# Kernel optimization log

Hardware: AMD Instinct MI355X
Metric: run time of the kernel (lower is better)

Reference implementation:

```python
import jax, jax.numpy as jnp
import numpy as np

EPS = 1e-5  # BatchNorm eps (torch default)


def _coords():
    # coord_tensor[i] = [(i//5 - 2)/2, (i%5 - 2)/2] for 5x5 grid of 25 objects
    i = jnp.arange(25)
    return jnp.stack([(i // 5 - 2) / 2.0, (i % 5 - 2) / 2.0], axis=-1).astype(jnp.float32)


def _conv_bn(x, w, b, gamma, beta):
    # conv stride2 pad1 -> relu -> batchnorm (training-mode batch stats, as torch module default)
    y = jax.lax.conv_general_dilated(x, w, (2, 2), ((1, 1), (1, 1)),
                                     dimension_numbers=('NCHW', 'OIHW', 'NCHW'))
    y = jax.nn.relu(y + b[None, :, None, None])
    m = y.mean(axis=(0, 2, 3), keepdims=True)
    v = y.var(axis=(0, 2, 3), keepdims=True)
    return gamma[None, :, None, None] * (y - m) * jax.lax.rsqrt(v + EPS) + beta[None, :, None, None]


def setup_inputs() -> dict:
    key = jax.random.key(0)
    ks = iter(jax.random.split(key, 64))
    def rn(shape, scale=0.05):
        return jax.random.normal(next(ks), shape, jnp.float32) * scale
    B = 256
    inp = {
        'x': jax.random.normal(next(ks), (B, 3, 80, 80), jnp.float32),
        'qst': jax.random.normal(next(ks), (B, 11), jnp.float32),
    }
    for l, (ci, co) in enumerate([(3, 24), (24, 24), (24, 24), (24, 24)], 1):
        inp[f'cw{l}'] = rn((co, ci, 3, 3))
        inp[f'cb{l}'] = jnp.zeros((co,), jnp.float32)
        inp[f'bg{l}'] = jnp.ones((co,), jnp.float32)
        inp[f'bb{l}'] = jnp.zeros((co,), jnp.float32)
    for l, (di, do) in enumerate([(63, 256), (256, 256), (256, 256), (256, 256)], 1):
        inp[f'gw{l}'] = rn((di, do))
        inp[f'gb{l}'] = jnp.zeros((do,), jnp.float32)
    for l, (di, do) in enumerate([(256, 256), (256, 256), (256, 10)], 1):
        inp[f'fw{l}'] = rn((di, do))
        inp[f'fb{l}'] = jnp.zeros((do,), jnp.float32)
    return inp


def _forward(x, qst, cw1, cb1, bg1, bb1, cw2, cb2, bg2, bb2,
             cw3, cb3, bg3, bb3, cw4, cb4, bg4, bb4,
             gw1, gb1, gw2, gb2, gw3, gb3, gw4, gb4,
             fw1, fb1, fw2, fb2, fw3, fb3):
    B = x.shape[0]
    # Convolution stack: (B,3,80,80) -> (B,24,5,5)
    h = _conv_bn(x, cw1, cb1, bg1, bb1)
    h = _conv_bn(h, cw2, cb2, bg2, bb2)
    h = _conv_bn(h, cw3, cb3, bg3, bb3)
    h = _conv_bn(h, cw4, cb4, bg4, bb4)
    # Objects: (B,24,25) -> (B,25,24) -> concat coords -> (B,25,26)
    obj = h.reshape(B, 24, 25).transpose(0, 2, 1)
    obj = jnp.concatenate([obj, jnp.broadcast_to(_coords()[None], (B, 25, 2))], axis=-1)
    # Pairwise broadcast-concat: cat([x_i, x_j, qst]) with x_i[b,p,q]=obj[b,q], x_j[b,p,q]=obj[b,p]
    xi = jnp.broadcast_to(obj[:, None, :, :], (B, 25, 25, 26))
    xj = jnp.broadcast_to(obj[:, :, None, :], (B, 25, 25, 26))
    qb = jnp.broadcast_to(qst[:, None, None, :], (B, 25, 25, 11))
    pairs = jnp.concatenate([xi, xj, qb], axis=-1).reshape(B, 625, 63)
    g = jax.nn.relu(pairs @ gw1 + gb1)
    g = jax.nn.relu(g @ gw2 + gb2)
    g = jax.nn.relu(g @ gw3 + gb3)
    g = jax.nn.relu(g @ gw4 + gb4).sum(axis=1)  # (B,256)
    # f_phi (dropout treated as identity for a deterministic reference)
    f = jax.nn.relu(g @ fw1 + fb1)
    f = jax.nn.relu(f @ fw2 + fb2)
    logits = f @ fw3 + fb3
    return jax.nn.log_softmax(logits, axis=1)


def reference(x, qst, cw1, cb1, bg1, bb1, cw2, cb2, bg2, bb2,
              cw3, cb3, bg3, bb3, cw4, cb4, bg4, bb4,
              gw1, gb1, gw2, gb2, gw3, gb3, gw4, gb4,
              fw1, fb1, fw2, fb2, fw3, fb3):
    return _forward(x, qst, cw1, cb1, bg1, bb1, cw2, cb2, bg2, bb2,
                    cw3, cb3, bg3, bb3, cw4, cb4, bg4, bb4,
                    gw1, gb1, gw2, gb2, gw3, gb3, gw4, gb4,
                    fw1, fb1, fw2, fb2, fw3, fb3)
```

## Files before the change

kernel.cpp:

```cpp
#include <hip/hip_runtime.h>
#include <hip/hip_bf16.h>


typedef __attribute__((ext_vector_type(8))) short short8;
typedef __attribute__((ext_vector_type(4))) float floatx4;

__device__ __forceinline__ unsigned short f2bf(float v){
  union { float f; unsigned int u; } c; c.f = v;
  unsigned int u = c.u;
  u += 0x7FFFu + ((u >> 16) & 1u);
  return (unsigned short)(u >> 16);
}

__global__ __launch_bounds__(256) void prep_w_zero(
    const float* __restrict__ gw2, const float* __restrict__ gw3,
    const float* __restrict__ gw4, unsigned short* __restrict__ wf,
    float* __restrict__ stats)
{
  const int bid = blockIdx.x, tid = threadIdx.x;
  if (bid == 0){ for (int j = tid; j < 1536; j += 256) stats[j] = 0.f; }
  const int w = bid >> 8;
  const float* gw = (w == 0) ? gw2 : (w == 1) ? gw3 : gw4;
  const int idx = (bid & 255)*256 + tid;
  const int i = idx & 7, lane = (idx >> 3) & 63, t = (idx >> 9) & 15, kk = idx >> 13;
  const int k = kk*32 + (lane >> 4)*8 + i;
  const int c = t*16 + (lane & 15);
  wf[w*65536 + idx] = f2bf(gw[k*256 + c]);
}

template<int CI, int COG, int PX>
__global__ __launch_bounds__(256) void conv_px(
    const float* __restrict__ in,
    const float* __restrict__ stats_in, const float* __restrict__ gprev,
    const float* __restrict__ bprev, float invN,
    const float* __restrict__ cw, const float* __restrict__ cb,
    float* __restrict__ out, float* __restrict__ stats_out,
    int H, int W, int OH, int OW)
{
  const int co0 = blockIdx.y * COG;
  __shared__ float ssm[2*CI];
  __shared__ float psum[4][COG], psum2[4][COG];
  const int tid = threadIdx.x;
  if (tid < CI){
    if (stats_in){
      float S = 0.f, S2 = 0.f;
      #pragma unroll
      for (int sh = 0; sh < 8; sh++){ S += stats_in[sh*48 + tid]; S2 += stats_in[sh*48 + 24 + tid]; }
      const float mean = S*invN;
      const float var  = S2*invN - mean*mean;
      const float rs   = rsqrtf(var + 1e-5f);
      const float sc   = gprev[tid]*rs;
      ssm[tid] = sc; ssm[CI + tid] = bprev[tid] - mean*sc;
    } else { ssm[tid] = 1.f; ssm[CI + tid] = 0.f; }
  }
  __syncthreads();
  const int nw = OW / PX;
  const int idx = blockIdx.x*256 + tid;
  const int pw = idx % nw; const int t2 = idx / nw;
  const int oh = t2 % OH;  const int b  = t2 / OH;
  const int ow0 = pw * PX;
  const float* cwb = cw + co0*CI*9;
  constexpr int NC = 2*PX + 1;
  float acc[PX][COG];
  #pragma unroll
  for (int j = 0; j < PX; j++)
    #pragma unroll
    for (int g = 0; g < COG; g++) acc[j][g] = cb[co0 + g];

  #pragma unroll 1
  for (int ci = 0; ci < CI; ci++){
    const float* ip = in + ((long)(b*CI + ci))*H*W;
    const float sc = ssm[ci], sh2 = ssm[CI + ci];
    float v[3][NC];
    #pragma unroll
    for (int kh = 0; kh < 3; kh++){
      const int ih = oh*2 - 1 + kh;
      const bool hok = (ih >= 0);
      #pragma unroll
      for (int c9 = 0; c9 < NC; c9++){
        const int iw = ow0*2 - 1 + c9;
        const bool ok = hok & (iw >= 0);
        const float raw = ip[ok ? ih*W + iw : 0];
        v[kh][c9] = ok ? raw*sc + sh2 : 0.f;
      }
    }
    #pragma unroll
    for (int g = 0; g < COG; g++){
      #pragma unroll
      for (int kh = 0; kh < 3; kh++){
        const float w0 = cwb[(g*CI + ci)*9 + kh*3 + 0];
        const float w1 = cwb[(g*CI + ci)*9 + kh*3 + 1];
        const float w2 = cwb[(g*CI + ci)*9 + kh*3 + 2];
        #pragma unroll
        for (int j = 0; j < PX; j++)
          acc[j][g] += v[kh][2*j]*w0 + v[kh][2*j+1]*w1 + v[kh][2*j+2]*w2;
      }
    }
  }

  const int wave = tid >> 6, lane = tid & 63;
  float s[COG], s2[COG];
  #pragma unroll
  for (int g = 0; g < COG; g++){
    float tmp[PX], a = 0.f, a2 = 0.f;
    #pragma unroll
    for (int j = 0; j < PX; j++){
      tmp[j] = fmaxf(acc[j][g], 0.f);
      a += tmp[j]; a2 += tmp[j]*tmp[j];
    }
    float* op = &out[(((long)b*24 + co0 + g)*OH + oh)*OW + ow0];
    if constexpr (PX == 4) *(float4*)op = make_float4(tmp[0], tmp[1], tmp[2], tmp[3]);
    else if constexpr (PX == 2) *(float2*)op = make_float2(tmp[0], tmp[1]);
    else op[0] = tmp[0];
    s[g] = a; s2[g] = a2;
  }
  #pragma unroll
  for (int g = 0; g < COG; g++){
    float a = s[g], a2 = s2[g];
    for (int off = 32; off; off >>= 1){ a += __shfl_down(a, off); a2 += __shfl_down(a2, off); }
    if (lane == 0){ psum[wave][g] = a; psum2[wave][g] = a2; }
  }
  __syncthreads();
  if (tid < COG){
    const float S  = psum[0][tid] + psum[1][tid] + psum[2][tid] + psum[3][tid];
    const float S2 = psum2[0][tid] + psum2[1][tid] + psum2[2][tid] + psum2[3][tid];
    const int sh = blockIdx.x & 7;
    atomicAdd(&stats_out[sh*48 + co0 + tid],      S);
    atomicAdd(&stats_out[sh*48 + 24 + co0 + tid], S2);
  }
}

__global__ __launch_bounds__(512) void g_mega(
    const float* __restrict__ y4, const float* __restrict__ stats4,
    const float* __restrict__ bg4, const float* __restrict__ bb4,
    const float* __restrict__ qst, const float* __restrict__ gw1,
    const float* __restrict__ gb1,
    const unsigned short* __restrict__ Wf,
    const float* __restrict__ gb2, const float* __restrict__ gb3, const float* __restrict__ gb4,
    const float* __restrict__ fw1, const float* __restrict__ fb1,
    const float* __restrict__ fw2, const float* __restrict__ fb2,
    const float* __restrict__ fw3, const float* __restrict__ fb3,
    float* __restrict__ out)
{
  __shared__ __align__(16) short act[128*256];
  __shared__ __align__(16) float A_lds[25][260];
  __shared__ __align__(16) float Bm_lds[25][260];
  __shared__ float obj[25][26];
  __shared__ float ssum[48];
  __shared__ float ssm[48];
  __shared__ float scratch[512];
  __shared__ __align__(16) float bufA[256], bufB[256];
  __shared__ float lg[10];

  const int b = blockIdx.x, tid = threadIdx.x;
  char* actB = (char*)act;
  const int wave = tid >> 6, lane = tid & 63;
  const int lmod = lane & 15, ldiv = lane >> 4;
  const int wm = wave >> 2, wn = wave & 3;

  if (tid < 48){
    float S = 0.f;
    #pragma unroll
    for (int sh = 0; sh < 8; sh++) S += stats4[sh*48 + tid];
    ssum[tid] = S;
  }
  __syncthreads();
  if (tid < 24){
    const float mean = ssum[tid]*(1.f/6400.f);
    const float var  = ssum[24 + tid]*(1.f/6400.f) - mean*mean;
    const float rs   = rsqrtf(var + 1e-5f);
    const float sc   = bg4[tid]*rs;
    ssm[tid] = sc; ssm[24 + tid] = bb4[tid] - mean*sc;
  }
  __syncthreads();
  for (int j = tid; j < 600; j += 512){
    const int q = j/24, c = j%24;
    obj[q][c] = ssm[c]*y4[((long)(b*24 + c))*25 + q] + ssm[24 + c];
  }
  if (tid < 50){
    const int q = tid >> 1;
    obj[q][24 + (tid & 1)] = (tid & 1) ? (float)(q%5 - 2)*0.5f : (float)(q/5 - 2)*0.5f;
  }
  __syncthreads();
  {
    const int n = tid & 255, half = tid >> 8;
    float wa[26], wb[26];
    #pragma unroll
    for (int c = 0; c < 26; c++){ wa[c] = gw1[c*256 + n]; wb[c] = gw1[(26 + c)*256 + n]; }
    float qv = gb1[n];
    #pragma unroll
    for (int j = 0; j < 11; j++) qv += qst[b*11 + j]*gw1[(52 + j)*256 + n];
    const int q0 = half ? 13 : 0, q1 = half ? 25 : 13;
    for (int q = q0; q < q1; q++){
      float a = qv, bm = 0.f;
      #pragma unroll
      for (int c = 0; c < 26; c++){ const float o = obj[q][c]; a += o*wa[c]; bm += o*wb[c]; }
      A_lds[q][n] = a; Bm_lds[q][n] = bm;
    }
  }
  __syncthreads();

  float gsum = 0.f;
  for (int blk = 0; blk < 5; blk++){
    const int rowbase = blk * 128;
    const int nrows = min(128, 625 - rowbase);
    {
      const int r  = tid >> 2;
      const int q4 = tid & 3;
      if (r < nrows){
        const int row = rowbase + r;
        const float* ap = &A_lds [row % 25][q4*4];
        const float* bp = &Bm_lds[row / 25][q4*4];
        #pragma unroll
        for (int j = 0; j < 16; j++){
          const int c = j*16;
          floatx4 av = *(const floatx4*)(ap + c);
          floatx4 bv = *(const floatx4*)(bp + c);
          unsigned int p0 = (unsigned int)f2bf(fmaxf(av.x+bv.x, 0.f))
                          | ((unsigned int)f2bf(fmaxf(av.y+bv.y, 0.f)) << 16);
          unsigned int p1 = (unsigned int)f2bf(fmaxf(av.z+bv.z, 0.f))
                          | ((unsigned int)f2bf(fmaxf(av.w+bv.w, 0.f)) << 16);
          const int byte = (r*512 + (c + q4*4)*2) ^ ((r & 7) << 4);
          *(uint2*)(actB + byte) = make_uint2(p0, p1);
        }
      } else {
        #pragma unroll
        for (int j = 0; j < 16; j++){
          const int byte = (r*512 + (j*16 + q4*4)*2) ^ ((r & 7) << 4);
          *(uint2*)(actB + byte) = make_uint2(0u, 0u);
        }
      }
    }
    __syncthreads();

    for (int L = 0; L < 3; L++){
      floatx4 acc[4][4];
      #pragma unroll
      for (int m = 0; m < 4; m++)
        #pragma unroll
        for (int n = 0; n < 4; n++)
          acc[m][n] = (floatx4){0.f,0.f,0.f,0.f};
      const short8* wlayer = (const short8*)Wf + (long)L*8192;
      #pragma unroll
      for (int kk = 0; kk < 8; kk++){
        short8 bf[4];
        #pragma unroll
        for (int n = 0; n < 4; n++)
          bf[n] = wlayer[(kk*16 + wn*4 + n)*64 + lane];
        short8 af[4];
        #pragma unroll
        for (int m = 0; m < 4; m++){
          const int arow  = wm*64 + m*16 + lmod;
          const int abyte = (arow*512 + kk*64 + ldiv*16) ^ ((arow & 7) << 4);
          af[m] = *(const short8*)(actB + abyte);
        }
        #pragma unroll
        for (int n = 0; n < 4; n++)
          #pragma unroll
          for (int m = 0; m < 4; m++)
            acc[m][n] = __builtin_amdgcn_mfma_f32_16x16x32_bf16(af[m], bf[n], acc[m][n], 0, 0, 0);
      }

      if (L < 2){
        const float* bias = (L == 0) ? gb2 : gb3;
        __syncthreads();
        #pragma unroll
        for (int n = 0; n < 4; n++){
          const int c = (wn*4 + n)*16 + lmod;
          const float bv = bias[c];
          #pragma unroll
          for (int m = 0; m < 4; m++){
            #pragma unroll
            for (int i = 0; i < 4; i++){
              const int row = wm*64 + m*16 + ldiv*4 + i;
              const float v = fmaxf(acc[m][n][i] + bv, 0.f);
              const int byte = (row*512 + c*2) ^ ((row & 7) << 4);
              *(short*)(actB + byte) = (short)f2bf(v);
            }
          }
        }
        __syncthreads();
      } else {
        __syncthreads();
        #pragma unroll
        for (int n = 0; n < 4; n++){
          const int c = (wn*4 + n)*16 + lmod;
          const float bv = gb4[c];
          float sv = 0.f;
          #pragma unroll
          for (int m = 0; m < 4; m++){
            #pragma unroll
            for (int i = 0; i < 4; i++){
              const int row = wm*64 + m*16 + ldiv*4 + i;
              const float v = fmaxf(acc[m][n][i] + bv, 0.f);
              if (row < nrows) sv += v;
            }
          }
          sv += __shfl_xor(sv, 16);
          sv += __shfl_xor(sv, 32);
          if (ldiv == 0) scratch[wm*256 + c] = sv;
        }
        __syncthreads();
        if (tid < 256) gsum += scratch[tid] + scratch[256 + tid];
      }
    }
  }

  if (tid < 256) bufA[tid] = gsum;
  __syncthreads();
  const int n = tid & 255;
  float acc = 0.f;
  if (tid < 256){
    acc = fb1[n];
    const float4* pa = (const float4*)bufA;
    #pragma unroll 8
    for (int k4 = 0; k4 < 64; k4++){
      const float4 a = pa[k4];
      acc += a.x*fw1[(k4*4 + 0)*256 + n];
      acc += a.y*fw1[(k4*4 + 1)*256 + n];
      acc += a.z*fw1[(k4*4 + 2)*256 + n];
      acc += a.w*fw1[(k4*4 + 3)*256 + n];
    }
    bufB[n] = fmaxf(acc, 0.f);
  }
  __syncthreads();
  if (tid < 256){
    acc = fb2[n];
    const float4* pb = (const float4*)bufB;
    #pragma unroll 8
    for (int k4 = 0; k4 < 64; k4++){
      const float4 a = pb[k4];
      acc += a.x*fw2[(k4*4 + 0)*256 + n];
      acc += a.y*fw2[(k4*4 + 1)*256 + n];
      acc += a.z*fw2[(k4*4 + 2)*256 + n];
      acc += a.w*fw2[(k4*4 + 3)*256 + n];
    }
  }
  __syncthreads();
  if (tid < 256) bufA[n] = fmaxf(acc, 0.f);
  __syncthreads();
  if (tid < 10){
    float a3 = fb3[tid];
    for (int k = 0; k < 256; k++) a3 += bufA[k]*fw3[k*10 + tid];
    lg[tid] = a3;
  }
  __syncthreads();
  if (tid < 10){
    float m = lg[0];
    #pragma unroll
    for (int j = 1; j < 10; j++) m = fmaxf(m, lg[j]);
    float s = 0.f;
    #pragma unroll
    for (int j = 0; j < 10; j++) s += expf(lg[j] - m);
    out[b*10 + tid] = lg[tid] - m - logf(s);
  }
}

extern "C" void kernel_launch(void* const* d_in, const int* in_sizes, int n_in,
                              void* d_out, int out_size, void* d_ws, size_t ws_size,
                              hipStream_t stream)
{
  const float* x   = (const float*)d_in[0];
  const float* qst = (const float*)d_in[1];
  const float* cw1 = (const float*)d_in[2];
  const float* cb1 = (const float*)d_in[3];
  const float* bg1 = (const float*)d_in[4];
  const float* bb1 = (const float*)d_in[5];
  const float* cw2 = (const float*)d_in[6];
  const float* cb2 = (const float*)d_in[7];
  const float* bg2 = (const float*)d_in[8];
  const float* bb2 = (const float*)d_in[9];
  const float* cw3 = (const float*)d_in[10];
  const float* cb3 = (const float*)d_in[11];
  const float* bg3 = (const float*)d_in[12];
  const float* bb3 = (const float*)d_in[13];
  const float* cw4 = (const float*)d_in[14];
  const float* cb4 = (const float*)d_in[15];
  const float* bg4 = (const float*)d_in[16];
  const float* bb4 = (const float*)d_in[17];
  const float* gw1 = (const float*)d_in[18];
  const float* gb1 = (const float*)d_in[19];
  const float* gw2 = (const float*)d_in[20];
  const float* gb2 = (const float*)d_in[21];
  const float* gw3 = (const float*)d_in[22];
  const float* gb3 = (const float*)d_in[23];
  const float* gw4 = (const float*)d_in[24];
  const float* gb4 = (const float*)d_in[25];
  const float* fw1 = (const float*)d_in[26];
  const float* fb1 = (const float*)d_in[27];
  const float* fw2 = (const float*)d_in[28];
  const float* fb2 = (const float*)d_in[29];
  const float* fw3 = (const float*)d_in[30];
  const float* fb3 = (const float*)d_in[31];

  float* wsf    = (float*)d_ws;
  unsigned short* Wf = (unsigned short*)(wsf + 65728);
  float* stats  = wsf + 164032;
  float* y1     = wsf + 240832;
  float* y2     = wsf + 10071232;
  float* y3     = wsf + 12528832;
  float* y4     = wsf + 13143232;

  prep_w_zero<<<768, 256, 0, stream>>>(gw2, gw3, gw4, Wf, stats);
  conv_px<3,8,4><<<dim3(400,3), 256, 0, stream>>>(x, nullptr, nullptr, nullptr, 0.f,
                                               cw1, cb1, y1, stats + 0, 80,80,40,40);
  conv_px<24,8,4><<<dim3(100,3), 256, 0, stream>>>(y1, stats + 0, bg1, bb1, 1.f/409600.f,
                                               cw2, cb2, y2, stats + 384, 40,40,20,20);
  conv_px<24,8,2><<<dim3(50,3), 256, 0, stream>>>(y2, stats + 384, bg2, bb2, 1.f/102400.f,
                                               cw3, cb3, y3, stats + 768, 20,20,10,10);
  conv_px<24,8,1><<<dim3(25,3), 256, 0, stream>>>(y3, stats + 768, bg3, bb3, 1.f/25600.f,
                                              cw4, cb4, y4, stats + 1152, 10,10,5,5);
  g_mega<<<256, 512, 0, stream>>>(y4, stats + 1152, bg4, bb4, qst, gw1, gb1, Wf,
                                  gb2, gb3, gb4, fw1, fb1, fw2, fb2, fw3, fb3,
                                  (float*)d_out);
}
```

Measured before the change: 288.9 us.

## Fuse weight prep into conv1 and replace atomic BN stats with per-block partials

```diff
diff --git a/kernel.cpp b/kernel.cpp
--- a/kernel.cpp
+++ b/kernel.cpp
@@ -12,46 +12,124 @@
   return (unsigned short)(u >> 16);
 }
 
-__global__ __launch_bounds__(256) void prep_w_zero(
+__global__ __launch_bounds__(256) void conv1_fat(
     const float* __restrict__ gw2, const float* __restrict__ gw3,
     const float* __restrict__ gw4, unsigned short* __restrict__ wf,
-    float* __restrict__ stats)
+    const float* __restrict__ x, const float* __restrict__ cw1,
+    const float* __restrict__ cb1,
+    float* __restrict__ out, float* __restrict__ pstats1)
 {
   const int bid = blockIdx.x, tid = threadIdx.x;
-  if (bid == 0){ for (int j = tid; j < 1536; j += 256) stats[j] = 0.f; }
-  const int w = bid >> 8;
-  const float* gw = (w == 0) ? gw2 : (w == 1) ? gw3 : gw4;
-  const int idx = (bid & 255)*256 + tid;
-  const int i = idx & 7, lane = (idx >> 3) & 63, t = (idx >> 9) & 15, kk = idx >> 13;
-  const int k = kk*32 + (lane >> 4)*8 + i;
-  const int c = t*16 + (lane & 15);
-  wf[w*65536 + idx] = f2bf(gw[k*256 + c]);
+  if (bid < 768){
+    const int w = bid >> 8;
+    const float* gw = (w == 0) ? gw2 : (w == 1) ? gw3 : gw4;
+    const int idx = (bid & 255)*256 + tid;
+    const int i = idx & 7, lane = (idx >> 3) & 63, t = (idx >> 9) & 15, kk = idx >> 13;
+    const int k = kk*32 + (lane >> 4)*8 + i;
+    const int c = t*16 + (lane & 15);
+    wf[w*65536 + idx] = f2bf(gw[k*256 + c]);
+    return;
+  }
+  __shared__ float psum[4][8], psum2[4][8];
+  const int cb = bid - 768;
+  const int grp = cb / 400, xb = cb % 400;
+  const int co0 = grp * 8;
+  const int idx = xb*256 + tid;
+  const int pw = idx % 10; const int t2 = idx / 10;
+  const int oh = t2 % 40;  const int b  = t2 / 40;
+  const int ow0 = pw * 4;
+  const float* cwb = cw1 + co0*3*9;
+  float acc[4][8];
+  #pragma unroll
+  for (int j = 0; j < 4; j++)
+    #pragma unroll
+    for (int g = 0; g < 8; g++) acc[j][g] = cb1[co0 + g];
+  #pragma unroll
+  for (int ci = 0; ci < 3; ci++){
+    const float* ip = x + ((long)(b*3 + ci))*6400;
+    float v[3][9];
+    #pragma unroll
+    for (int kh = 0; kh < 3; kh++){
+      const int ih = oh*2 - 1 + kh;
+      const bool hok = (ih >= 0);
+      #pragma unroll
+      for (int c9 = 0; c9 < 9; c9++){
+        const int iw = ow0*2 - 1 + c9;
+        const bool ok = hok & (iw >= 0);
+        v[kh][c9] = ok ? ip[ok ? ih*80 + iw : 0] : 0.f;
+      }
+    }
+    #pragma unroll
+    for (int g = 0; g < 8; g++){
+      #pragma unroll
+      for (int kh = 0; kh < 3; kh++){
+        const float w0 = cwb[(g*3 + ci)*9 + kh*3 + 0];
+        const float w1 = cwb[(g*3 + ci)*9 + kh*3 + 1];
+        const float w2 = cwb[(g*3 + ci)*9 + kh*3 + 2];
+        #pragma unroll
+        for (int j = 0; j < 4; j++)
+          acc[j][g] += v[kh][2*j]*w0 + v[kh][2*j+1]*w1 + v[kh][2*j+2]*w2;
+      }
+    }
+  }
+  const int wave = tid >> 6, lane = tid & 63;
+  float s[8], s2[8];
+  #pragma unroll
+  for (int g = 0; g < 8; g++){
+    float tmp[4], a = 0.f, a2 = 0.f;
+    #pragma unroll
+    for (int j = 0; j < 4; j++){
+      tmp[j] = fmaxf(acc[j][g], 0.f);
+      a += tmp[j]; a2 += tmp[j]*tmp[j];
+    }
+    *(float4*)&out[(((long)b*24 + co0 + g)*40 + oh)*40 + ow0] =
+        make_float4(tmp[0], tmp[1], tmp[2], tmp[3]);
+    s[g] = a; s2[g] = a2;
+  }
+  #pragma unroll
+  for (int g = 0; g < 8; g++){
+    float a = s[g], a2 = s2[g];
+    for (int off = 32; off; off >>= 1){ a += __shfl_down(a, off); a2 += __shfl_down(a2, off); }
+    if (lane == 0){ psum[wave][g] = a; psum2[wave][g] = a2; }
+  }
+  __syncthreads();
+  if (tid < 8){
+    pstats1[(co0 + tid)*400 + xb]      = psum[0][tid] + psum[1][tid] + psum[2][tid] + psum[3][tid];
+    pstats1[(24 + co0 + tid)*400 + xb] = psum2[0][tid] + psum2[1][tid] + psum2[2][tid] + psum2[3][tid];
+  }
 }
 
-template<int CI, int COG, int PX>
+template<int CI, int COG, int PX, int NIN, int NOUT>
 __global__ __launch_bounds__(256) void conv_px(
-    const float* __restrict__ in,
-    const float* __restrict__ stats_in, const float* __restrict__ gprev,
-    const float* __restrict__ bprev, float invN,
+    const float* __restrict__ in, const float* __restrict__ pst_in,
+    const float* __restrict__ gprev, const float* __restrict__ bprev, float invN,
     const float* __restrict__ cw, const float* __restrict__ cb,
-    float* __restrict__ out, float* __restrict__ stats_out,
+    float* __restrict__ out, float* __restrict__ pst_out,
     int H, int W, int OH, int OW)
 {
   const int co0 = blockIdx.y * COG;
+  __shared__ float psub[48][5];
   __shared__ float ssm[2*CI];
   __shared__ float psum[4][COG], psum2[4][COG];
   const int tid = threadIdx.x;
-  if (tid < CI){
-    if (stats_in){
-      float S = 0.f, S2 = 0.f;
-      #pragma unroll
-      for (int sh = 0; sh < 8; sh++){ S += stats_in[sh*48 + tid]; S2 += stats_in[sh*48 + 24 + tid]; }
-      const float mean = S*invN;
-      const float var  = S2*invN - mean*mean;
-      const float rs   = rsqrtf(var + 1e-5f);
-      const float sc   = gprev[tid]*rs;
-      ssm[tid] = sc; ssm[CI + tid] = bprev[tid] - mean*sc;
-    } else { ssm[tid] = 1.f; ssm[CI + tid] = 0.f; }
+  if (tid < 240){
+    const int c = tid / 5, sub = tid % 5;
+    constexpr int chunk = NIN / 5;
+    const float* p = pst_in + c*NIN + sub*chunk;
+    float S0 = 0.f, S1 = 0.f;
+    #pragma unroll 2
+    for (int j = 0; j < chunk; j += 2){ S0 += p[j]; S1 += p[j+1]; }
+    psub[c][sub] = S0 + S1;
+  }
+  __syncthreads();
+  if (tid < 24){
+    const float Sm  = psub[tid][0] + psub[tid][1] + psub[tid][2] + psub[tid][3] + psub[tid][4];
+    const float S2m = psub[24+tid][0] + psub[24+tid][1] + psub[24+tid][2] + psub[24+tid][3] + psub[24+tid][4];
+    const float mean = Sm*invN;
+    const float var  = S2m*invN - mean*mean;
+    const float rs   = rsqrtf(var + 1e-5f);
+    const float sc   = gprev[tid]*rs;
+    ssm[tid] = sc; ssm[CI + tid] = bprev[tid] - mean*sc;
   }
   __syncthreads();
   const int nw = OW / PX;
@@ -122,16 +200,13 @@
   }
   __syncthreads();
   if (tid < COG){
-    const float S  = psum[0][tid] + psum[1][tid] + psum[2][tid] + psum[3][tid];
-    const float S2 = psum2[0][tid] + psum2[1][tid] + psum2[2][tid] + psum2[3][tid];
-    const int sh = blockIdx.x & 7;
-    atomicAdd(&stats_out[sh*48 + co0 + tid],      S);
-    atomicAdd(&stats_out[sh*48 + 24 + co0 + tid], S2);
+    pst_out[(co0 + tid)*NOUT + blockIdx.x]      = psum[0][tid] + psum[1][tid] + psum[2][tid] + psum[3][tid];
+    pst_out[(24 + co0 + tid)*NOUT + blockIdx.x] = psum2[0][tid] + psum2[1][tid] + psum2[2][tid] + psum2[3][tid];
   }
 }
 
 __global__ __launch_bounds__(512) void g_mega(
-    const float* __restrict__ y4, const float* __restrict__ stats4,
+    const float* __restrict__ y4, const float* __restrict__ pstats4,
     const float* __restrict__ bg4, const float* __restrict__ bb4,
     const float* __restrict__ qst, const float* __restrict__ gw1,
     const float* __restrict__ gb1,
@@ -160,8 +235,9 @@
 
   if (tid < 48){
     float S = 0.f;
-    #pragma unroll
-    for (int sh = 0; sh < 8; sh++) S += stats4[sh*48 + tid];
+    const float* p = pstats4 + tid*25;
+    #pragma unroll
+    for (int j = 0; j < 25; j++) S += p[j];
     ssum[tid] = S;
   }
   __syncthreads();
@@ -393,24 +469,25 @@
   const float* fw3 = (const float*)d_in[30];
   const float* fb3 = (const float*)d_in[31];
 
-  float* wsf    = (float*)d_ws;
+  float* wsf     = (float*)d_ws;
+  float* pstats1 = wsf + 0;
+  float* pstats2 = wsf + 19200;
+  float* pstats3 = wsf + 24000;
+  float* pstats4 = wsf + 26400;
   unsigned short* Wf = (unsigned short*)(wsf + 65728);
-  float* stats  = wsf + 164032;
-  float* y1     = wsf + 240832;
-  float* y2     = wsf + 10071232;
-  float* y3     = wsf + 12528832;
-  float* y4     = wsf + 13143232;
-
-  prep_w_zero<<<768, 256, 0, stream>>>(gw2, gw3, gw4, Wf, stats);
-  conv_px<3,8,4><<<dim3(400,3), 256, 0, stream>>>(x, nullptr, nullptr, nullptr, 0.f,
-                                               cw1, cb1, y1, stats + 0, 80,80,40,40);
-  conv_px<24,8,4><<<dim3(100,3), 256, 0, stream>>>(y1, stats + 0, bg1, bb1, 1.f/409600.f,
-                                               cw2, cb2, y2, stats + 384, 40,40,20,20);
-  conv_px<24,8,2><<<dim3(50,3), 256, 0, stream>>>(y2, stats + 384, bg2, bb2, 1.f/102400.f,
-                                               cw3, cb3, y3, stats + 768, 20,20,10,10);
-  conv_px<24,8,1><<<dim3(25,3), 256, 0, stream>>>(y3, stats + 768, bg3, bb3, 1.f/25600.f,
-                                              cw4, cb4, y4, stats + 1152, 10,10,5,5);
-  g_mega<<<256, 512, 0, stream>>>(y4, stats + 1152, bg4, bb4, qst, gw1, gb1, Wf,
+  float* y1      = wsf + 240832;
+  float* y2      = wsf + 10071232;
+  float* y3      = wsf + 12528832;
+  float* y4      = wsf + 13143232;
+
+  conv1_fat<<<1968, 256, 0, stream>>>(gw2, gw3, gw4, Wf, x, cw1, cb1, y1, pstats1);
+  conv_px<24,8,4,400,100><<<dim3(100,3), 256, 0, stream>>>(
+      y1, pstats1, bg1, bb1, 1.f/409600.f, cw2, cb2, y2, pstats2, 40,40,20,20);
+  conv_px<24,8,2,100,50><<<dim3(50,3), 256, 0, stream>>>(
+      y2, pstats2, bg2, bb2, 1.f/102400.f, cw3, cb3, y3, pstats3, 20,20,10,10);
+  conv_px<24,8,1,50,25><<<dim3(25,3), 256, 0, stream>>>(
+      y3, pstats3, bg3, bb3, 1.f/25600.f, cw4, cb4, y4, pstats4, 10,10,5,5);
+  g_mega<<<256, 512, 0, stream>>>(y4, pstats4, bg4, bb4, qst, gw1, gb1, Wf,
                                   gb2, gb3, gb4, fw1, fb1, fw2, fb2, fw3, fb3,
                                   (float*)d_out);
 }
```

Result: faster. 271.3 us, median of 2 (-6.1%).
